# Kernel tuning notes

Measured on AMD Instinct MI355X. Metric: run time of the kernel, lower is better.

## Reference

```python
import jax, jax.numpy as jnp
import numpy as np

N_NODES = 100000
N_EDGES = 1600000
N_PAIRS = 1000000
IN_CH = 32
HID = 32


def glorot(key, shape):
    lim = float(np.sqrt(6.0 / (shape[0] + shape[1])))
    return jax.random.uniform(key, shape, jnp.float32, -lim, lim)


def setup_inputs() -> dict:
    key = jax.random.key(0)
    ks = jax.random.split(key, 9)
    x = jax.random.normal(ks[0], (N_NODES, IN_CH), jnp.float32)
    edge_index = jax.random.randint(ks[1], (2, N_EDGES), 0, N_NODES, jnp.int64)
    edge_pairs = jax.random.randint(ks[2], (N_PAIRS, 2), 0, N_NODES, jnp.int64)
    # SAGEConv params: lin_l acts on aggregated neighbors (has bias), lin_r on root.
    Wl1 = glorot(ks[3], (IN_CH, HID)); Wr1 = glorot(ks[4], (IN_CH, HID)); b1 = jnp.zeros((HID,), jnp.float32)
    Wl2 = glorot(ks[5], (HID, HID)); Wr2 = glorot(ks[6], (HID, HID)); b2 = jnp.zeros((HID,), jnp.float32)
    return {"x": x, "edge_index": edge_index, "edge_pairs": edge_pairs,
            "Wl1": Wl1, "Wr1": Wr1, "b1": b1, "Wl2": Wl2, "Wr2": Wr2, "b2": b2}


def sage_conv(x, src, dst, Wl, Wr, b):
    # mean-aggregate messages x[src] at dst, then linear + root linear
    msgs = x[src]                                             # [E, d] gather
    agg = jax.ops.segment_sum(msgs, dst, num_segments=N_NODES)  # [N, d]
    cnt = jax.ops.segment_sum(jnp.ones((src.shape[0],), x.dtype), dst, num_segments=N_NODES)
    agg = agg / jnp.maximum(cnt, 1.0)[:, None]
    return agg @ Wl + b + x @ Wr


def reference(x, edge_index, edge_pairs, Wl1, Wr1, b1, Wl2, Wr2, b2):
    src, dst = edge_index[0], edge_index[1]
    h = jax.nn.relu(sage_conv(x, src, dst, Wl1, Wr1, b1))  # dropout is identity in eval
    z = sage_conv(h, src, dst, Wl2, Wr2, b2)               # [N, HID]
    logits = jnp.sum(z[edge_pairs[:, 0]] * z[edge_pairs[:, 1]], axis=-1)  # [num_pairs]
    return logits
```

## Files before the change

kernel.cpp:

```cpp
#include <hip/hip_runtime.h>

typedef unsigned short ushort_t;
typedef unsigned int uint_t;

#define N_NODES 100000
#define N_EDGES 1600000
#define N_PAIRS 1000000
#define BSHIFT 9
#define BUCKET (1 << BSHIFT)
#define NBUCKET ((N_NODES + BUCKET - 1) >> BSHIFT)
#define SC_T 512
#define SC_K 8
#define EPB (SC_T * SC_K)

__device__ __forceinline__ float bf2f(ushort_t u) {
    return __uint_as_float(((unsigned)u) << 16);
}
__device__ __forceinline__ ushort_t f2bf(float f) {
    unsigned u = __float_as_uint(f);
    return (ushort_t)((u + 0x7FFFu + ((u >> 16) & 1u)) >> 16);
}

__global__ void cvt_kernel(const float* __restrict__ in, ushort_t* __restrict__ out) {
    int i = blockIdx.x * blockDim.x + threadIdx.x;
    if (i < N_NODES * 8) {
        float4 v = ((const float4*)in)[i];
        ushort4 o;
        o.x = f2bf(v.x); o.y = f2bf(v.y); o.z = f2bf(v.z); o.w = f2bf(v.w);
        ((ushort4*)out)[i] = o;
    }
}

__global__ void bhist_kernel(const int* __restrict__ dst, int* __restrict__ ghist) {
    __shared__ int hist[NBUCKET];
    int t = threadIdx.x;
    for (int i = t; i < NBUCKET; i += blockDim.x) hist[i] = 0;
    __syncthreads();
    long long e0 = (long long)blockIdx.x * EPB;
    long long e1 = e0 + EPB;
    if (e1 > N_EDGES) e1 = N_EDGES;
    for (long long i = e0 + t; i < e1; i += blockDim.x)
        atomicAdd(&hist[dst[i] >> BSHIFT], 1);
    __syncthreads();
    for (int i = t; i < NBUCKET; i += blockDim.x)
        if (hist[i]) atomicAdd(&ghist[i], hist[i]);
}

__global__ void bscan_kernel(const int* __restrict__ ghist, int* __restrict__ boff,
                             int* __restrict__ bcursor, int* __restrict__ offsets) {
    __shared__ int tmp[256];
    int t = threadIdx.x;
    tmp[t] = (t < NBUCKET) ? ghist[t] : 0;
    __syncthreads();
    for (int off = 1; off < 256; off <<= 1) {
        int v = (t >= off) ? tmp[t - off] : 0;
        __syncthreads();
        tmp[t] += v;
        __syncthreads();
    }
    int excl = (t > 0) ? tmp[t - 1] : 0;
    if (t < NBUCKET) { boff[t] = excl; bcursor[t] = excl; }
    if (t == NBUCKET) {
        boff[t] = excl;
        offsets[N_NODES] = excl;
    }
}

__global__ void bscatter_kernel(const int* __restrict__ src,
                                const int* __restrict__ dst,
                                int* __restrict__ bcursor,
                                int* __restrict__ bed) {
    __shared__ int hist[NBUCKET];
    __shared__ int base[NBUCKET];
    __shared__ int stage[EPB];
    __shared__ unsigned char sbkt[EPB];
    int t = threadIdx.x;
    long long e0 = (long long)blockIdx.x * EPB;
    int cnt = (int)((N_EDGES - e0 < EPB) ? (N_EDGES - e0) : EPB);

    for (int i = t; i < NBUCKET; i += SC_T) hist[i] = 0;
    __syncthreads();
    for (int i = t; i < cnt; i += SC_T) {
        int s = src[e0 + i];
        int d = dst[e0 + i];
        int b = d >> BSHIFT;
        stage[i] = (s << BSHIFT) | (d & (BUCKET - 1));
        sbkt[i] = (unsigned char)b;
        atomicAdd(&hist[b], 1);
    }
    __syncthreads();
    for (int i = t; i < NBUCKET; i += SC_T) {
        int c = hist[i];
        base[i] = c ? atomicAdd(&bcursor[i], c) : 0;
        hist[i] = 0;
    }
    __syncthreads();
    for (int i = t; i < cnt; i += SC_T) {
        int b = sbkt[i];
        int r = atomicAdd(&hist[b], 1);
        bed[base[b] + r] = stage[i];
    }
}

__global__ void ffill_kernel(const int* __restrict__ bed,
                             const int* __restrict__ boff,
                             int* __restrict__ offsets,
                             int* __restrict__ csr) {
    __shared__ int cnt[BUCKET];
    __shared__ int scn[BUCKET];
    __shared__ int cur[BUCKET];
    int b = blockIdx.x;
    int t = threadIdx.x;
    int base = boff[b], bend = boff[b + 1];

    if (t < BUCKET) cnt[t] = 0;
    __syncthreads();
    for (int i = base + t; i < bend; i += blockDim.x)
        atomicAdd(&cnt[bed[i] & (BUCKET - 1)], 1);
    __syncthreads();
    if (t < BUCKET) scn[t] = cnt[t];
    __syncthreads();
    for (int off = 1; off < BUCKET; off <<= 1) {
        int v = 0;
        if (t < BUCKET && t >= off) v = scn[t - off];
        __syncthreads();
        if (t < BUCKET) scn[t] += v;
        __syncthreads();
    }
    if (t < BUCKET) {
        int excl = scn[t] - cnt[t];
        cur[t] = base + excl;
        int n = (b << BSHIFT) + t;
        if (n < N_NODES) offsets[n] = base + excl;
    }
    __syncthreads();
    for (int i = base + t; i < bend; i += blockDim.x) {
        int p = bed[i];
        int pos = atomicAdd(&cur[p & (BUCKET - 1)], 1);
        csr[pos] = p >> BSHIFT;
    }
}

template <bool RELU, bool ROOT16>
__global__ void agg_linear_kernel(const ushort_t* __restrict__ feat16,
                                  const float* __restrict__ feat32,
                                  const int* __restrict__ csr,
                                  const int* __restrict__ offs,
                                  const float* __restrict__ Wl,
                                  const float* __restrict__ Wr,
                                  const float* __restrict__ b,
                                  ushort_t* __restrict__ out16) {
    __shared__ float sWl[1024], sWr[1024], sb[32];
    for (int i = threadIdx.x; i < 1024; i += blockDim.x) {
        sWl[i] = Wl[i];
        sWr[i] = Wr[i];
    }
    if (threadIdx.x < 32) sb[threadIdx.x] = b[threadIdx.x];
    __syncthreads();

    int g = threadIdx.x >> 5;
    int c = threadIdx.x & 31;
    int n = blockIdx.x * 8 + g;
    if (n >= N_NODES) return;

    const ushort_t* fc = feat16 + c;
    int beg = offs[n], end = offs[n + 1];
    float a0 = 0.f, a1 = 0.f, a2 = 0.f, a3 = 0.f;
    float a4 = 0.f, a5 = 0.f, a6 = 0.f, a7 = 0.f;
    int j = beg;
    for (; j + 7 < end; j += 8) {
        int s0 = csr[j + 0], s1 = csr[j + 1], s2 = csr[j + 2], s3 = csr[j + 3];
        int s4 = csr[j + 4], s5 = csr[j + 5], s6 = csr[j + 6], s7 = csr[j + 7];
        a0 += bf2f(fc[s0 * 32]); a1 += bf2f(fc[s1 * 32]);
        a2 += bf2f(fc[s2 * 32]); a3 += bf2f(fc[s3 * 32]);
        a4 += bf2f(fc[s4 * 32]); a5 += bf2f(fc[s5 * 32]);
        a6 += bf2f(fc[s6 * 32]); a7 += bf2f(fc[s7 * 32]);
    }
    for (; j < end; j++) a0 += bf2f(fc[csr[j] * 32]);
    float inv = 1.0f / (float)max(end - beg, 1);
    float acc = (((a0 + a1) + (a2 + a3)) + ((a4 + a5) + (a6 + a7))) * inv;
    float xr = ROOT16 ? bf2f(fc[n * 32]) : feat32[(long long)n * 32 + c];

    float o = sb[c];
#pragma unroll
    for (int i = 0; i < 32; i++) {
        float ai = __shfl(acc, i, 32);
        float xi = __shfl(xr, i, 32);
        o += ai * sWl[i * 32 + c] + xi * sWr[i * 32 + c];
    }
    float r = RELU ? fmaxf(o, 0.f) : o;
    out16[(long long)n * 32 + c] = f2bf(r);
}

__global__ void pair_kernel(const ushort_t* __restrict__ z16,
                            const int* __restrict__ pairs,
                            float* __restrict__ out) {
    int gid = blockIdx.x * blockDim.x + threadIdx.x;
    int q = gid >> 3;
    int l = gid & 7;
    if (q >= N_PAIRS / 4) return;
    const int4* pp = (const int4*)pairs;
    int4 i01 = pp[2 * q];
    int4 i23 = pp[2 * q + 1];
    const ushort_t* zl = z16 + l * 4;
    ushort4 a0 = *(const ushort4*)(zl + (long long)i01.x * 32);
    ushort4 b0 = *(const ushort4*)(zl + (long long)i01.y * 32);
    ushort4 a1 = *(const ushort4*)(zl + (long long)i01.z * 32);
    ushort4 b1 = *(const ushort4*)(zl + (long long)i01.w * 32);
    ushort4 a2 = *(const ushort4*)(zl + (long long)i23.x * 32);
    ushort4 b2 = *(const ushort4*)(zl + (long long)i23.y * 32);
    ushort4 a3 = *(const ushort4*)(zl + (long long)i23.z * 32);
    ushort4 b3 = *(const ushort4*)(zl + (long long)i23.w * 32);
    float d0 = bf2f(a0.x) * bf2f(b0.x) + bf2f(a0.y) * bf2f(b0.y)
             + bf2f(a0.z) * bf2f(b0.z) + bf2f(a0.w) * bf2f(b0.w);
    float d1 = bf2f(a1.x) * bf2f(b1.x) + bf2f(a1.y) * bf2f(b1.y)
             + bf2f(a1.z) * bf2f(b1.z) + bf2f(a1.w) * bf2f(b1.w);
    float d2 = bf2f(a2.x) * bf2f(b2.x) + bf2f(a2.y) * bf2f(b2.y)
             + bf2f(a2.z) * bf2f(b2.z) + bf2f(a2.w) * bf2f(b2.w);
    float d3 = bf2f(a3.x) * bf2f(b3.x) + bf2f(a3.y) * bf2f(b3.y)
             + bf2f(a3.z) * bf2f(b3.z) + bf2f(a3.w) * bf2f(b3.w);
#pragma unroll
    for (int off = 4; off >= 1; off >>= 1) {
        d0 += __shfl_xor(d0, off, 8);
        d1 += __shfl_xor(d1, off, 8);
        d2 += __shfl_xor(d2, off, 8);
        d3 += __shfl_xor(d3, off, 8);
    }
    if (l < 4) {
        float v = (l == 0) ? d0 : (l == 1) ? d1 : (l == 2) ? d2 : d3;
        out[4 * q + l] = v;
    }
}

extern "C" void kernel_launch(void* const* d_in, const int* in_sizes, int n_in,
                              void* d_out, int out_size, void* d_ws, size_t ws_size,
                              hipStream_t stream) {
    const float* x   = (const float*)d_in[0];
    const int*   ei  = (const int*)d_in[1];
    const int*   prs = (const int*)d_in[2];
    const float* Wl1 = (const float*)d_in[3];
    const float* Wr1 = (const float*)d_in[4];
    const float* b1  = (const float*)d_in[5];
    const float* Wl2 = (const float*)d_in[6];
    const float* Wr2 = (const float*)d_in[7];
    const float* b2  = (const float*)d_in[8];
    float* out = (float*)d_out;

    const int* src = ei;
    const int* dst = ei + N_EDGES;

    ushort_t* x16 = (ushort_t*)d_ws;
    ushort_t* h16 = x16 + (size_t)N_NODES * 32;
    ushort_t* z16 = h16 + (size_t)N_NODES * 32;
    int* csr      = (int*)(z16 + (size_t)N_NODES * 32);
    int* offsets  = csr + N_EDGES;
    int* ghist    = offsets + (N_NODES + 1);
    int* boff     = ghist + NBUCKET;
    int* bcursor  = boff + (NBUCKET + 1);
    int* bed      = (int*)z16;

    const int BT = 256;
    int cvt_blocks  = (N_NODES * 8 + BT - 1) / BT;
    int bsc_blocks  = (N_EDGES + EPB - 1) / EPB;
    int agg_blocks  = (N_NODES + 7) / 8;
    int pair_blocks = (int)(((long long)N_PAIRS * 2 + BT - 1) / BT);

    hipMemsetAsync(ghist, 0, sizeof(int) * NBUCKET, stream);
    cvt_kernel<<<cvt_blocks, BT, 0, stream>>>(x, x16);
    bhist_kernel<<<bsc_blocks, BT, 0, stream>>>(dst, ghist);
    bscan_kernel<<<1, 256, 0, stream>>>(ghist, boff, bcursor, offsets);
    bscatter_kernel<<<bsc_blocks, SC_T, 0, stream>>>(src, dst, bcursor, bed);
    ffill_kernel<<<NBUCKET, 1024, 0, stream>>>(bed, boff, offsets, csr);

    agg_linear_kernel<true, false><<<agg_blocks, BT, 0, stream>>>(
        x16, x, csr, offsets, Wl1, Wr1, b1, h16);
    agg_linear_kernel<false, true><<<agg_blocks, BT, 0, stream>>>(
        h16, nullptr, csr, offsets, Wl2, Wr2, b2, z16);

    pair_kernel<<<pair_blocks, BT, 0, stream>>>(z16, prs, out);
}
```

Measured before the change: 309.7 us.

## Split features into two 16-channel halves to shrink gather working sets

```diff
diff --git a/kernel.cpp b/kernel.cpp
--- a/kernel.cpp
+++ b/kernel.cpp
@@ -20,15 +20,35 @@
     unsigned u = __float_as_uint(f);
     return (ushort_t)((u + 0x7FFFu + ((u >> 16) & 1u)) >> 16);
 }
-
-__global__ void cvt_kernel(const float* __restrict__ in, ushort_t* __restrict__ out) {
-    int i = blockIdx.x * blockDim.x + threadIdx.x;
-    if (i < N_NODES * 8) {
-        float4 v = ((const float4*)in)[i];
-        ushort4 o;
-        o.x = f2bf(v.x); o.y = f2bf(v.y); o.z = f2bf(v.z); o.w = f2bf(v.w);
-        ((ushort4*)out)[i] = o;
-    }
+__device__ __forceinline__ uint_t pk2(float a, float b) {
+    return (uint_t)f2bf(a) | ((uint_t)f2bf(b) << 16);
+}
+__device__ __forceinline__ void load_bf16_half(const ushort_t* __restrict__ p, float* X) {
+    const uint4* rp = (const uint4*)p;
+#pragma unroll
+    for (int k = 0; k < 2; k++) {
+        uint4 r = rp[k];
+        uint_t u;
+        u = r.x; X[8 * k + 0] = __uint_as_float(u << 16); X[8 * k + 1] = __uint_as_float(u & 0xFFFF0000u);
+        u = r.y; X[8 * k + 2] = __uint_as_float(u << 16); X[8 * k + 3] = __uint_as_float(u & 0xFFFF0000u);
+        u = r.z; X[8 * k + 4] = __uint_as_float(u << 16); X[8 * k + 5] = __uint_as_float(u & 0xFFFF0000u);
+        u = r.w; X[8 * k + 6] = __uint_as_float(u << 16); X[8 * k + 7] = __uint_as_float(u & 0xFFFF0000u);
+    }
+}
+
+__global__ void cvt_kernel(const float* __restrict__ in,
+                           ushort_t* __restrict__ outA,
+                           ushort_t* __restrict__ outB) {
+    int t = blockIdx.x * blockDim.x + threadIdx.x;
+    if (t >= 2 * N_NODES) return;
+    int n = t >> 1, h = t & 1;
+    const float4* p = (const float4*)(in + (long long)n * 32 + h * 16);
+    float4 v0 = p[0], v1 = p[1], v2 = p[2], v3 = p[3];
+    uint4 o0 = make_uint4(pk2(v0.x, v0.y), pk2(v0.z, v0.w), pk2(v1.x, v1.y), pk2(v1.z, v1.w));
+    uint4 o1 = make_uint4(pk2(v2.x, v2.y), pk2(v2.z, v2.w), pk2(v3.x, v3.y), pk2(v3.z, v3.w));
+    uint4* o = (uint4*)((h ? outB : outA) + (long long)n * 16);
+    o[0] = o0;
+    o[1] = o1;
 }
 
 __global__ void bhist_kernel(const int* __restrict__ dst, int* __restrict__ ghist) {
@@ -141,29 +161,16 @@
     }
 }
 
-template <bool RELU, bool ROOT16>
-__global__ void agg_linear_kernel(const ushort_t* __restrict__ feat16,
-                                  const float* __restrict__ feat32,
-                                  const int* __restrict__ csr,
-                                  const int* __restrict__ offs,
-                                  const float* __restrict__ Wl,
-                                  const float* __restrict__ Wr,
-                                  const float* __restrict__ b,
-                                  ushort_t* __restrict__ out16) {
-    __shared__ float sWl[1024], sWr[1024], sb[32];
-    for (int i = threadIdx.x; i < 1024; i += blockDim.x) {
-        sWl[i] = Wl[i];
-        sWr[i] = Wr[i];
-    }
-    if (threadIdx.x < 32) sb[threadIdx.x] = b[threadIdx.x];
-    __syncthreads();
-
-    int g = threadIdx.x >> 5;
-    int c = threadIdx.x & 31;
-    int n = blockIdx.x * 8 + g;
+__global__ void gather16_kernel(const ushort_t* __restrict__ featH,
+                                const int* __restrict__ csr,
+                                const int* __restrict__ offs,
+                                ushort_t* __restrict__ aggH) {
+    int g = threadIdx.x >> 4;
+    int c = threadIdx.x & 15;
+    int n = blockIdx.x * 16 + g;
     if (n >= N_NODES) return;
 
-    const ushort_t* fc = feat16 + c;
+    const ushort_t* fc = featH + c;
     int beg = offs[n], end = offs[n + 1];
     float a0 = 0.f, a1 = 0.f, a2 = 0.f, a3 = 0.f;
     float a4 = 0.f, a5 = 0.f, a6 = 0.f, a7 = 0.f;
@@ -171,28 +178,96 @@
     for (; j + 7 < end; j += 8) {
         int s0 = csr[j + 0], s1 = csr[j + 1], s2 = csr[j + 2], s3 = csr[j + 3];
         int s4 = csr[j + 4], s5 = csr[j + 5], s6 = csr[j + 6], s7 = csr[j + 7];
-        a0 += bf2f(fc[s0 * 32]); a1 += bf2f(fc[s1 * 32]);
-        a2 += bf2f(fc[s2 * 32]); a3 += bf2f(fc[s3 * 32]);
-        a4 += bf2f(fc[s4 * 32]); a5 += bf2f(fc[s5 * 32]);
-        a6 += bf2f(fc[s6 * 32]); a7 += bf2f(fc[s7 * 32]);
-    }
-    for (; j < end; j++) a0 += bf2f(fc[csr[j] * 32]);
+        a0 += bf2f(fc[s0 * 16]); a1 += bf2f(fc[s1 * 16]);
+        a2 += bf2f(fc[s2 * 16]); a3 += bf2f(fc[s3 * 16]);
+        a4 += bf2f(fc[s4 * 16]); a5 += bf2f(fc[s5 * 16]);
+        a6 += bf2f(fc[s6 * 16]); a7 += bf2f(fc[s7 * 16]);
+    }
+    for (; j < end; j++) a0 += bf2f(fc[csr[j] * 16]);
     float inv = 1.0f / (float)max(end - beg, 1);
     float acc = (((a0 + a1) + (a2 + a3)) + ((a4 + a5) + (a6 + a7))) * inv;
-    float xr = ROOT16 ? bf2f(fc[n * 32]) : feat32[(long long)n * 32 + c];
-
-    float o = sb[c];
+    aggH[(long long)n * 16 + c] = f2bf(acc);
+}
+
+template <bool RELU, bool ROOT16>
+__global__ __launch_bounds__(256, 1) void linear_kernel(
+    const ushort_t* __restrict__ aggA, const ushort_t* __restrict__ aggB,
+    const ushort_t* __restrict__ rootA, const ushort_t* __restrict__ rootB,
+    const float* __restrict__ root32,
+    const float* __restrict__ Wl, const float* __restrict__ Wr,
+    const float* __restrict__ b,
+    ushort_t* __restrict__ outA, ushort_t* __restrict__ outB) {
+    __shared__ float4 sWl[256], sWr[256], sbv[8];
+    int t = threadIdx.x;
+    if (t < 256) {
+        sWl[t] = ((const float4*)Wl)[t];
+        sWr[t] = ((const float4*)Wr)[t];
+    }
+    if (t < 8) sbv[t] = ((const float4*)b)[t];
+    __syncthreads();
+
+    int n = blockIdx.x * blockDim.x + t;
+    if (n >= N_NODES) return;
+
+    float A[32];
+    load_bf16_half(aggA + (long long)n * 16, A);
+    load_bf16_half(aggB + (long long)n * 16, A + 16);
+
+    float X[32];
+    if (ROOT16) {
+        load_bf16_half(rootA + (long long)n * 16, X);
+        load_bf16_half(rootB + (long long)n * 16, X + 16);
+    } else {
+        const float4* rp = (const float4*)(root32 + (long long)n * 32);
+#pragma unroll
+        for (int q = 0; q < 8; q++) {
+            float4 v = rp[q];
+            X[4 * q + 0] = v.x; X[4 * q + 1] = v.y; X[4 * q + 2] = v.z; X[4 * q + 3] = v.w;
+        }
+    }
+
+    float4 O[8];
+#pragma unroll
+    for (int q = 0; q < 8; q++) O[q] = sbv[q];
+
 #pragma unroll
     for (int i = 0; i < 32; i++) {
-        float ai = __shfl(acc, i, 32);
-        float xi = __shfl(xr, i, 32);
-        o += ai * sWl[i * 32 + c] + xi * sWr[i * 32 + c];
-    }
-    float r = RELU ? fmaxf(o, 0.f) : o;
-    out16[(long long)n * 32 + c] = f2bf(r);
-}
-
-__global__ void pair_kernel(const ushort_t* __restrict__ z16,
+        float ai = A[i];
+        float xi = X[i];
+        const float4* wl = &sWl[i * 8];
+        const float4* wr = &sWr[i * 8];
+#pragma unroll
+        for (int q = 0; q < 8; q++) {
+            float4 wlv = wl[q];
+            float4 wrv = wr[q];
+            O[q].x += ai * wlv.x + xi * wrv.x;
+            O[q].y += ai * wlv.y + xi * wrv.y;
+            O[q].z += ai * wlv.z + xi * wrv.z;
+            O[q].w += ai * wlv.w + xi * wrv.w;
+        }
+    }
+
+    uint_t pk[16];
+#pragma unroll
+    for (int q = 0; q < 8; q++) {
+        float4 v = O[q];
+        if (RELU) {
+            v.x = fmaxf(v.x, 0.f); v.y = fmaxf(v.y, 0.f);
+            v.z = fmaxf(v.z, 0.f); v.w = fmaxf(v.w, 0.f);
+        }
+        pk[2 * q + 0] = pk2(v.x, v.y);
+        pk[2 * q + 1] = pk2(v.z, v.w);
+    }
+    uint4* oa = (uint4*)(outA + (long long)n * 16);
+    oa[0] = make_uint4(pk[0], pk[1], pk[2], pk[3]);
+    oa[1] = make_uint4(pk[4], pk[5], pk[6], pk[7]);
+    uint4* ob = (uint4*)(outB + (long long)n * 16);
+    ob[0] = make_uint4(pk[8], pk[9], pk[10], pk[11]);
+    ob[1] = make_uint4(pk[12], pk[13], pk[14], pk[15]);
+}
+
+template <bool ADD>
+__global__ void pair_kernel(const ushort_t* __restrict__ zH,
                             const int* __restrict__ pairs,
                             float* __restrict__ out) {
     int gid = blockIdx.x * blockDim.x + threadIdx.x;
@@ -202,23 +277,19 @@
     const int4* pp = (const int4*)pairs;
     int4 i01 = pp[2 * q];
     int4 i23 = pp[2 * q + 1];
-    const ushort_t* zl = z16 + l * 4;
-    ushort4 a0 = *(const ushort4*)(zl + (long long)i01.x * 32);
-    ushort4 b0 = *(const ushort4*)(zl + (long long)i01.y * 32);
-    ushort4 a1 = *(const ushort4*)(zl + (long long)i01.z * 32);
-    ushort4 b1 = *(const ushort4*)(zl + (long long)i01.w * 32);
-    ushort4 a2 = *(const ushort4*)(zl + (long long)i23.x * 32);
-    ushort4 b2 = *(const ushort4*)(zl + (long long)i23.y * 32);
-    ushort4 a3 = *(const ushort4*)(zl + (long long)i23.z * 32);
-    ushort4 b3 = *(const ushort4*)(zl + (long long)i23.w * 32);
-    float d0 = bf2f(a0.x) * bf2f(b0.x) + bf2f(a0.y) * bf2f(b0.y)
-             + bf2f(a0.z) * bf2f(b0.z) + bf2f(a0.w) * bf2f(b0.w);
-    float d1 = bf2f(a1.x) * bf2f(b1.x) + bf2f(a1.y) * bf2f(b1.y)
-             + bf2f(a1.z) * bf2f(b1.z) + bf2f(a1.w) * bf2f(b1.w);
-    float d2 = bf2f(a2.x) * bf2f(b2.x) + bf2f(a2.y) * bf2f(b2.y)
-             + bf2f(a2.z) * bf2f(b2.z) + bf2f(a2.w) * bf2f(b2.w);
-    float d3 = bf2f(a3.x) * bf2f(b3.x) + bf2f(a3.y) * bf2f(b3.y)
-             + bf2f(a3.z) * bf2f(b3.z) + bf2f(a3.w) * bf2f(b3.w);
+    const ushort_t* zl = zH + l * 2;
+    ushort2 a0 = *(const ushort2*)(zl + (long long)i01.x * 16);
+    ushort2 b0 = *(const ushort2*)(zl + (long long)i01.y * 16);
+    ushort2 a1 = *(const ushort2*)(zl + (long long)i01.z * 16);
+    ushort2 b1 = *(const ushort2*)(zl + (long long)i01.w * 16);
+    ushort2 a2 = *(const ushort2*)(zl + (long long)i23.x * 16);
+    ushort2 b2 = *(const ushort2*)(zl + (long long)i23.y * 16);
+    ushort2 a3 = *(const ushort2*)(zl + (long long)i23.z * 16);
+    ushort2 b3 = *(const ushort2*)(zl + (long long)i23.w * 16);
+    float d0 = bf2f(a0.x) * bf2f(b0.x) + bf2f(a0.y) * bf2f(b0.y);
+    float d1 = bf2f(a1.x) * bf2f(b1.x) + bf2f(a1.y) * bf2f(b1.y);
+    float d2 = bf2f(a2.x) * bf2f(b2.x) + bf2f(a2.y) * bf2f(b2.y);
+    float d3 = bf2f(a3.x) * bf2f(b3.x) + bf2f(a3.y) * bf2f(b3.y);
 #pragma unroll
     for (int off = 4; off >= 1; off >>= 1) {
         d0 += __shfl_xor(d0, off, 8);
@@ -228,7 +299,8 @@
     }
     if (l < 4) {
         float v = (l == 0) ? d0 : (l == 1) ? d1 : (l == 2) ? d2 : d3;
-        out[4 * q + l] = v;
+        int idx = 4 * q + l;
+        out[idx] = ADD ? (out[idx] + v) : v;
     }
 }
 
@@ -249,33 +321,45 @@
     const int* src = ei;
     const int* dst = ei + N_EDGES;
 
-    ushort_t* x16 = (ushort_t*)d_ws;
-    ushort_t* h16 = x16 + (size_t)N_NODES * 32;
-    ushort_t* z16 = h16 + (size_t)N_NODES * 32;
-    int* csr      = (int*)(z16 + (size_t)N_NODES * 32);
-    int* offsets  = csr + N_EDGES;
-    int* ghist    = offsets + (N_NODES + 1);
-    int* boff     = ghist + NBUCKET;
-    int* bcursor  = boff + (NBUCKET + 1);
-    int* bed      = (int*)z16;
+    ushort_t* xA   = (ushort_t*)d_ws;
+    ushort_t* xB   = xA + (size_t)N_NODES * 16;
+    ushort_t* hA   = xB + (size_t)N_NODES * 16;
+    ushort_t* hB   = hA + (size_t)N_NODES * 16;
+    ushort_t* aggA = hB + (size_t)N_NODES * 16;
+    ushort_t* aggB = aggA + (size_t)N_NODES * 16;
+    int* csr       = (int*)(aggB + (size_t)N_NODES * 16);
+    ushort_t* zA   = (ushort_t*)(csr + N_EDGES);
+    ushort_t* zB   = zA + (size_t)N_NODES * 16;
+    int* offsets   = (int*)(zB + (size_t)N_NODES * 16);
+    int* ghist     = offsets + (N_NODES + 1);
+    int* boff      = ghist + NBUCKET;
+    int* bcursor   = boff + (NBUCKET + 1);
+    int* bed       = (int*)zA;
 
     const int BT = 256;
-    int cvt_blocks  = (N_NODES * 8 + BT - 1) / BT;
+    int cvt_blocks  = (2 * N_NODES + BT - 1) / BT;
     int bsc_blocks  = (N_EDGES + EPB - 1) / EPB;
-    int agg_blocks  = (N_NODES + 7) / 8;
+    int g16_blocks  = (N_NODES + 15) / 16;
+    int lin_blocks  = (N_NODES + BT - 1) / BT;
     int pair_blocks = (int)(((long long)N_PAIRS * 2 + BT - 1) / BT);
 
     hipMemsetAsync(ghist, 0, sizeof(int) * NBUCKET, stream);
-    cvt_kernel<<<cvt_blocks, BT, 0, stream>>>(x, x16);
+    cvt_kernel<<<cvt_blocks, BT, 0, stream>>>(x, xA, xB);
     bhist_kernel<<<bsc_blocks, BT, 0, stream>>>(dst, ghist);
     bscan_kernel<<<1, 256, 0, stream>>>(ghist, boff, bcursor, offsets);
     bscatter_kernel<<<bsc_blocks, SC_T, 0, stream>>>(src, dst, bcursor, bed);
     ffill_kernel<<<NBUCKET, 1024, 0, stream>>>(bed, boff, offsets, csr);
 
-    agg_linear_kernel<true, false><<<agg_blocks, BT, 0, stream>>>(
-        x16, x, csr, offsets, Wl1, Wr1, b1, h16);
-    agg_linear_kernel<false, true><<<agg_blocks, BT, 0, stream>>>(
-        h16, nullptr, csr, offsets, Wl2, Wr2, b2, z16);
-
-    pair_kernel<<<pair_blocks, BT, 0, stream>>>(z16, prs, out);
-}
+    gather16_kernel<<<g16_blocks, BT, 0, stream>>>(xA, csr, offsets, aggA);
+    gather16_kernel<<<g16_blocks, BT, 0, stream>>>(xB, csr, offsets, aggB);
+    linear_kernel<true, false><<<lin_blocks, BT, 0, stream>>>(
+        aggA, aggB, nullptr, nullptr, x, Wl1, Wr1, b1, hA, hB);
+
+    gather16_kernel<<<g16_blocks, BT, 0, stream>>>(hA, csr, offsets, aggA);
+    gather16_kernel<<<g16_blocks, BT, 0, stream>>>(hB, csr, offsets, aggB);
+    linear_kernel<false, true><<<lin_blocks, BT, 0, stream>>>(
+        aggA, aggB, hA, hB, nullptr, Wl2, Wr2, b2, zA, zB);
+
+    pair_kernel<false><<<pair_blocks, BT, 0, stream>>>(zA, prs, out);
+    pair_kernel<true><<<pair_blocks, BT, 0, stream>>>(zB, prs, out);
+}
```

After: 303.0 us. 2.1% less time.
